# Optimization experiments

Measured on AMD Instinct MI355X. Metric: run time of the kernel, lower is better.

## Reference

```python
import jax, jax.numpy as jnp
import numpy as np

B, N, D, H = 2, 2048, 1024, 16
DK = D // H


def setup_inputs() -> dict:
    key = jax.random.key(0)
    ks = jax.random.split(key, 8)
    s = 1.0 / np.sqrt(D)  # keep projection outputs O(1)
    return {
        "x": jax.random.normal(ks[0], (B, N, D), jnp.float32),
        "alpha": jax.random.uniform(ks[1], (B, N), jnp.float32, -1.0, 1.0),
        "bias": jax.random.normal(ks[2], (B, N, N), jnp.float32) * 0.1,
        "Wq": jax.random.normal(ks[3], (D, D), jnp.float32) * s,
        "bq": jnp.zeros((D,), jnp.float32),
        "Wk": jax.random.normal(ks[4], (D, D), jnp.float32) * s,
        "bk": jnp.zeros((D,), jnp.float32),
        "Wv": jax.random.normal(ks[5], (D, D), jnp.float32) * s,
        "bv": jnp.zeros((D,), jnp.float32),
        "Wo": jax.random.normal(ks[6], (D, D), jnp.float32) * s,
        "bo": jnp.zeros((D,), jnp.float32),
    }


def reference(x, alpha, bias, Wq, bq, Wk, bk, Wv, bv, Wo, bo):
    b, n, d = x.shape
    # projections -> (B, H, N, DK)
    def split_heads(t):
        return t.reshape(b, n, H, DK).transpose(0, 2, 1, 3)

    q = split_heads(x @ Wq + bq)
    k = split_heads(x @ Wk + bk)
    v = split_heads(x @ Wv + bv)

    # salience rescale of keys/values: (B,1,N,1)
    scale = 1.0 + alpha[:, None, :, None]
    k = k * scale
    v = v * scale

    logits = jnp.einsum("bhnd,bhmd->bhnm", q, k) / np.float32(np.sqrt(DK))
    logits = logits + bias[:, None, :, :]  # broadcast over heads
    attn = jax.nn.softmax(logits, axis=-1)

    y = jnp.einsum("bhnm,bhmd->bhnd", attn, v)
    y = y.transpose(0, 2, 1, 3).reshape(b, n, d)
    return y @ Wo + bo
```

## Files before the change

### kernel.cpp

```cpp
#include <hip/hip_runtime.h>

typedef __attribute__((ext_vector_type(8))) short bf16x8;
typedef __attribute__((ext_vector_type(4))) float f32x4;

#define LOG2E 1.4426950408889634f

static __device__ __forceinline__ unsigned short f2bf(float f) {
    unsigned int u = __builtin_bit_cast(unsigned int, f);
    u += 0x7fffu + ((u >> 16) & 1u);
    return (unsigned short)(u >> 16);
}
static __device__ __forceinline__ void gload_lds16(const void* g, void* l) {
    __builtin_amdgcn_global_load_lds(
        (const __attribute__((address_space(1))) void*)g,
        (__attribute__((address_space(3))) void*)l, 16, 0, 0);
}

__launch_bounds__(256)
__global__ void prep(const float* __restrict__ x,
                     unsigned short* __restrict__ xb,
                     const float* __restrict__ W0, const float* __restrict__ W1,
                     const float* __restrict__ W2, const float* __restrict__ W3,
                     unsigned short* __restrict__ T0, unsigned short* __restrict__ T1,
                     unsigned short* __restrict__ T2, unsigned short* __restrict__ T3,
                     const float* __restrict__ bias,
                     unsigned short* __restrict__ biasP) {
    __shared__ __align__(16) float smem[8704];
    int id = blockIdx.x, tid = threadIdx.x;

    if (id < 2048) {
        int i = id * 256 + tid;
        const float4* s4 = (const float4*)x;
        float4 a = s4[2 * i], b = s4[2 * i + 1];
        uint4 u;
        u.x = (unsigned)f2bf(a.x) | ((unsigned)f2bf(a.y) << 16);
        u.y = (unsigned)f2bf(a.z) | ((unsigned)f2bf(a.w) << 16);
        u.z = (unsigned)f2bf(b.x) | ((unsigned)f2bf(b.y) << 16);
        u.w = (unsigned)f2bf(b.z) | ((unsigned)f2bf(b.w) << 16);
        *(uint4*)(xb + 8 * (size_t)i) = u;
        return;
    }
    if (id < 6144) {
        int j = id - 2048, which = j >> 10, r = j & 1023;
        const float* W = (which == 0) ? W0 : (which == 1) ? W1
                         : (which == 2) ? W2 : W3;
        unsigned short* Wt = (which == 0) ? T0 : (which == 1) ? T1
                             : (which == 2) ? T2 : T3;
        int tx = tid & 31, ty = tid >> 5;
        int x0 = (r & 31) * 32, y0 = (r >> 5) * 32;
        float* t = smem;
        for (int i = 0; i < 4; i++)
            t[(ty + 8 * i) * 33 + tx] =
                W[(size_t)(y0 + ty + 8 * i) * 1024 + x0 + tx];
        __syncthreads();
        for (int i = 0; i < 4; i++)
            Wt[(size_t)(x0 + ty + 8 * i) * 1024 + y0 + tx] =
                f2bf(t[tx * 33 + ty + 8 * i]);
        return;
    }
    {
        int j = id - 6144;
        int mt = j & 31, qt = (j >> 5) & 15, b = j >> 9;
        const float* s = bias + (size_t)b * 2048 * 2048;
        float* Ls = smem;
        for (int p = 0; p < 8; p++) {
            int row = p * 16 + (tid >> 4), f4 = tid & 15;
            float4 v = *(const float4*)
                &s[(size_t)(qt * 128 + row) * 2048 + mt * 64 + f4 * 4];
            *(float4*)&Ls[row * 68 + f4 * 4] = v;
        }
        __syncthreads();
        int w = tid >> 6, lane = tid & 63, quad = lane >> 4, l16 = lane & 15;
        unsigned short* d = biasP + (((size_t)(b * 16 + qt) * 32 + mt) * 8192);
        for (int e = 0; e < 2; e++) {
            unsigned short vals[16];
            for (int c = 0; c < 4; c++)
                for (int rr = 0; rr < 4; rr++)
                    vals[c * 4 + rr] =
                        f2bf(Ls[(e * 64 + w * 16 + quad * 4 + rr) * 68 +
                                c * 16 + l16] * LOG2E);
            unsigned short* o = d + ((size_t)((e * 4 + w) * 64 + lane)) * 16;
            *(bf16x8*)&o[0] = *(bf16x8*)&vals[0];
            *(bf16x8*)&o[8] = *(bf16x8*)&vals[8];
        }
    }
}

__launch_bounds__(256)
__global__ void gemm_qkv(const unsigned short* __restrict__ A,
                         const unsigned short* __restrict__ WqT,
                         const unsigned short* __restrict__ WkT,
                         const unsigned short* __restrict__ WvT,
                         const float* __restrict__ bq,
                         const float* __restrict__ bk,
                         const float* __restrict__ bv,
                         const float* __restrict__ alpha,
                         unsigned short* __restrict__ Qb,
                         unsigned short* __restrict__ Kb,
                         unsigned short* __restrict__ Vtb) {
    int which = blockIdx.y >> 3;
    const unsigned short* Bt = (which == 0) ? WqT : (which == 1) ? WkT : WvT;
    const float* bias = (which == 0) ? bq : (which == 1) ? bk : bv;

    __shared__ __align__(16) unsigned short As[128][64];
    __shared__ __align__(16) unsigned short Bs[128][64];
    int tid = threadIdx.x;
    int wave = tid >> 6, lane = tid & 63, quad = lane >> 4, l16 = lane & 15;
    int wm = wave & 1, wn = wave >> 1;
    int lrow = lane >> 3, lblk = lane & 7;
    int swz = ((lblk ^ lrow) * 8);
    int m0 = blockIdx.x * 128, n0 = (blockIdx.y & 7) * 128;
    f32x4 acc[4][4] = {};

    for (int kt = 0; kt < 16; kt++) {
        int k0 = kt * 64;
        for (int i = 0; i < 4; i++) {
            int rbase = i * 32 + wave * 8;
            gload_lds16(&A[(size_t)(m0 + rbase + lrow) * 1024 + k0 + swz],
                        &As[rbase][0]);
            gload_lds16(&Bt[(size_t)(n0 + rbase + lrow) * 1024 + k0 + swz],
                        &Bs[rbase][0]);
        }
        __syncthreads();
        for (int ks = 0; ks < 2; ks++) {
            int pblk = ((ks * 4 + quad) ^ (l16 & 7)) * 8;
            bf16x8 af[4], bf_[4];
            for (int i = 0; i < 4; i++)
                af[i] = *(const bf16x8*)&As[64 * wm + 16 * i + l16][pblk];
            for (int j = 0; j < 4; j++)
                bf_[j] = *(const bf16x8*)&Bs[64 * wn + 16 * j + l16][pblk];
            if (which == 2) {
                for (int i = 0; i < 4; i++)
                    for (int j = 0; j < 4; j++)
                        acc[i][j] = __builtin_amdgcn_mfma_f32_16x16x32_bf16(
                            af[i], bf_[j], acc[i][j], 0, 0, 0);
            } else {
                for (int i = 0; i < 4; i++)
                    for (int j = 0; j < 4; j++)
                        acc[i][j] = __builtin_amdgcn_mfma_f32_16x16x32_bf16(
                            bf_[j], af[i], acc[i][j], 0, 0, 0);
            }
        }
        __syncthreads();
    }

    if (which == 2) {
        for (int i = 0; i < 4; i++)
            for (int j = 0; j < 4; j++) {
                int colb = n0 + 64 * wn + 16 * j + l16;
                int h = colb >> 6, dk = colb & 63;
                int row0 = m0 + 64 * wm + 16 * i + quad * 4;
                int bb = row0 >> 11, nn0 = row0 & 2047;
                unsigned short v4[4];
                for (int r = 0; r < 4; r++) {
                    float v = acc[i][j][r] + bias[colb];
                    v4[r] = f2bf(v * (1.0f + alpha[bb * 2048 + nn0 + r]));
                }
                uint2 u;
                u.x = (unsigned)v4[0] | ((unsigned)v4[1] << 16);
                u.y = (unsigned)v4[2] | ((unsigned)v4[3] << 16);
                *(uint2*)&Vtb[((size_t)(bb * 16 + h) * 64 + dk) * 2048 + nn0] = u;
            }
    } else {
        unsigned short* outb = (which == 0) ? Qb : Kb;
        for (int i = 0; i < 4; i++)
            for (int j = 0; j < 4; j++) {
                int row = m0 + 64 * wm + 16 * i + l16;
                int bb = row >> 11, nn = row & 2047;
                int colb0 = n0 + 64 * wn + 16 * j + quad * 4;
                int h = colb0 >> 6, dk0 = colb0 & 63;
                float4 b4 = *(const float4*)&bias[colb0];
                float s = (which == 0) ? (0.125f * LOG2E)
                                       : (1.0f + alpha[bb * 2048 + nn]);
                unsigned short v4[4];
                v4[0] = f2bf((acc[i][j][0] + b4.x) * s);
                v4[1] = f2bf((acc[i][j][1] + b4.y) * s);
                v4[2] = f2bf((acc[i][j][2] + b4.z) * s);
                v4[3] = f2bf((acc[i][j][3] + b4.w) * s);
                uint2 u;
                u.x = (unsigned)v4[0] | ((unsigned)v4[1] << 16);
                u.y = (unsigned)v4[2] | ((unsigned)v4[3] << 16);
                *(uint2*)&outb[((size_t)(bb * 16 + h) * 2048 + nn) * 64 + dk0] = u;
            }
    }
}

__launch_bounds__(256)
__global__ void gemm_out(const unsigned short* __restrict__ A,
                         const unsigned short* __restrict__ Bt,
                         const float* __restrict__ bias,
                         float* __restrict__ outf) {
    __shared__ __align__(16) unsigned short As[128][64];
    __shared__ __align__(16) unsigned short Bs[128][64];
    int tid = threadIdx.x;
    int wave = tid >> 6, lane = tid & 63, quad = lane >> 4, l16 = lane & 15;
    int wm = wave & 1, wn = wave >> 1;
    int lrow = lane >> 3, lblk = lane & 7;
    int swz = ((lblk ^ lrow) * 8);
    int m0 = blockIdx.x * 128, n0 = blockIdx.y * 128;
    f32x4 acc[4][4] = {};

    for (int kt = 0; kt < 16; kt++) {
        int k0 = kt * 64;
        for (int i = 0; i < 4; i++) {
            int rbase = i * 32 + wave * 8;
            gload_lds16(&A[(size_t)(m0 + rbase + lrow) * 1024 + k0 + swz],
                        &As[rbase][0]);
            gload_lds16(&Bt[(size_t)(n0 + rbase + lrow) * 1024 + k0 + swz],
                        &Bs[rbase][0]);
        }
        __syncthreads();
        for (int ks = 0; ks < 2; ks++) {
            int pblk = ((ks * 4 + quad) ^ (l16 & 7)) * 8;
            bf16x8 af[4], bf_[4];
            for (int i = 0; i < 4; i++)
                af[i] = *(const bf16x8*)&As[64 * wm + 16 * i + l16][pblk];
            for (int j = 0; j < 4; j++)
                bf_[j] = *(const bf16x8*)&Bs[64 * wn + 16 * j + l16][pblk];
            for (int i = 0; i < 4; i++)
                for (int j = 0; j < 4; j++)
                    acc[i][j] = __builtin_amdgcn_mfma_f32_16x16x32_bf16(
                        bf_[j], af[i], acc[i][j], 0, 0, 0);
        }
        __syncthreads();
    }

    for (int i = 0; i < 4; i++)
        for (int j = 0; j < 4; j++) {
            int row = m0 + 64 * wm + 16 * i + l16;
            int colb0 = n0 + 64 * wn + 16 * j + quad * 4;
            float4 b4 = *(const float4*)&bias[colb0];
            float4 o;
            o.x = acc[i][j][0] + b4.x;
            o.y = acc[i][j][1] + b4.y;
            o.z = acc[i][j][2] + b4.z;
            o.w = acc[i][j][3] + b4.w;
            *(float4*)&outf[(size_t)row * 1024 + colb0] = o;
        }
}

__launch_bounds__(256, 4)
__global__ void attn_kernel(const unsigned short* __restrict__ Q,
                            const unsigned short* __restrict__ K,
                            const unsigned short* __restrict__ Vt,
                            const unsigned short* __restrict__ biasP,
                            unsigned short* __restrict__ Y,
                            float* __restrict__ Opart,
                            float* __restrict__ Lpart, int split) {
    __shared__ __align__(16) unsigned short Ks[64][64];
    __shared__ __align__(16) unsigned short Vs[64][64];
    __shared__ __align__(16) unsigned short Ps[4][32][72];
    int tid = threadIdx.x;
    int wave = tid >> 6, lane = tid & 63, quad = lane >> 4, l16 = lane & 15;
    int qt = blockIdx.x, h = blockIdx.y;
    int b, mt0, mtN;
    if (split) { b = blockIdx.z >> 1; int half = blockIdx.z & 1;
                 mt0 = half * 16; mtN = mt0 + 16; }
    else       { b = blockIdx.z; mt0 = 0; mtN = 32; }
    int q0 = qt * 128;
    size_t headoff = (size_t)(b * 16 + h) * 2048 * 64;
    const unsigned short* Kp = K + headoff;
    const unsigned short* Vp = Vt + headoff;
    int lrow = lane >> 3, lblk = lane & 7;
    int swz = (lblk ^ lrow) * 8;

    bf16x8 aq[2][2];
    for (int e = 0; e < 2; e++) {
        const unsigned short* qp =
            Q + headoff + (size_t)(q0 + e * 64 + wave * 16 + l16) * 64;
        aq[e][0] = *(const bf16x8*)&qp[quad * 8];
        aq[e][1] = *(const bf16x8*)&qp[32 + quad * 8];
    }
    bf16x8 ones;
    for (int j = 0; j < 8; j++) ones[j] = (short)0x3F80;

    f32x4 oacc[2][4] = {};
    f32x4 lacc[2] = {};
    const unsigned short* bP = biasP + (size_t)(b * 16 + qt) * 32 * 8192;

    for (int mt = mt0; mt < mtN; mt++) {
        int m0 = mt * 64;
        for (int i = 0; i < 2; i++) {
            int rbase = wave * 16 + i * 8;
            gload_lds16(&Kp[(size_t)(m0 + rbase + lrow) * 64 + swz], &Ks[rbase][0]);
            gload_lds16(&Vp[(size_t)(rbase + lrow) * 2048 + m0 + swz], &Vs[rbase][0]);
        }
        const unsigned short* bt = bP + (size_t)mt * 8192;
        bf16x8 bz[2][2];
        for (int e = 0; e < 2; e++) {
            const unsigned short* p = bt + (size_t)((e * 4 + wave) * 64 + lane) * 16;
            bz[e][0] = *(const bf16x8*)&p[0];
            bz[e][1] = *(const bf16x8*)&p[8];
        }
        __syncthreads();

        f32x4 sc[2][4];
        for (int e = 0; e < 2; e++)
            for (int c = 0; c < 4; c++) {
                uint2 w = ((const uint2*)&bz[e][c >> 1])[c & 1];
                f32x4 s;
                s[0] = __builtin_bit_cast(float, w.x << 16);
                s[1] = __builtin_bit_cast(float, w.x & 0xffff0000u);
                s[2] = __builtin_bit_cast(float, w.y << 16);
                s[3] = __builtin_bit_cast(float, w.y & 0xffff0000u);
                sc[e][c] = s;
            }
        __builtin_amdgcn_s_setprio(1);
        for (int c = 0; c < 4; c++) {
            for (int ks = 0; ks < 2; ks++) {
                bf16x8 kf = *(const bf16x8*)&Ks[c * 16 + l16]
                                               [((ks * 4 + quad) ^ (l16 & 7)) * 8];
                sc[0][c] = __builtin_amdgcn_mfma_f32_16x16x32_bf16(aq[0][ks], kf, sc[0][c], 0, 0, 0);
                sc[1][c] = __builtin_amdgcn_mfma_f32_16x16x32_bf16(aq[1][ks], kf, sc[1][c], 0, 0, 0);
            }
        }
        __builtin_amdgcn_s_setprio(0);

        for (int e = 0; e < 2; e++)
            for (int c = 0; c < 4; c++) {
                int colw = (((c * 2 + (l16 >> 3)) + quad) & 7) * 8 + (l16 & 7);
                for (int r = 0; r < 4; r++) {
                    float p = exp2f(sc[e][c][r]);
                    unsigned int u = __builtin_bit_cast(unsigned int, p);
                    Ps[wave][e * 16 + quad * 4 + r][colw] = (unsigned short)(u >> 16);
                }
            }

        __builtin_amdgcn_s_setprio(1);
        for (int ks = 0; ks < 2; ks++) {
            int blkr = (ks * 4 + quad + (l16 >> 2)) & 7;
            bf16x8 pf0 = *(const bf16x8*)&Ps[wave][l16][blkr * 8];
            bf16x8 pf1 = *(const bf16x8*)&Ps[wave][16 + l16][blkr * 8];
            lacc[0] = __builtin_amdgcn_mfma_f32_16x16x32_bf16(pf0, ones, lacc[0], 0, 0, 0);
            lacc[1] = __builtin_amdgcn_mfma_f32_16x16x32_bf16(pf1, ones, lacc[1], 0, 0, 0);
            for (int cv = 0; cv < 4; cv++) {
                bf16x8 vf = *(const bf16x8*)&Vs[cv * 16 + l16]
                                               [((ks * 4 + quad) ^ (l16 & 7)) * 8];
                oacc[0][cv] = __builtin_amdgcn_mfma_f32_16x16x32_bf16(pf0, vf, oacc[0][cv], 0, 0, 0);
                oacc[1][cv] = __builtin_amdgcn_mfma_f32_16x16x32_bf16(pf1, vf, oacc[1][cv], 0, 0, 0);
            }
        }
        __builtin_amdgcn_s_setprio(0);
        __syncthreads();
    }

    if (split) {
        size_t p = ((size_t)((b * 16 + h) * 16 + qt)) * 2 + (blockIdx.z & 1);
        float* Op = Opart + p * 8192;
        for (int e = 0; e < 2; e++)
            for (int cv = 0; cv < 4; cv++)
                for (int r = 0; r < 4; r++)
                    Op[(e * 64 + wave * 16 + quad * 4 + r) * 64 + cv * 16 + l16] =
                        oacc[e][cv][r];
        if (l16 == 0)
            for (int e = 0; e < 2; e++)
                for (int r = 0; r < 4; r++)
                    Lpart[p * 128 + e * 64 + wave * 16 + quad * 4 + r] = lacc[e][r];
    } else {
        for (int e = 0; e < 2; e++) {
            float invl[4];
            for (int r = 0; r < 4; r++) invl[r] = 1.0f / lacc[e][r];
            for (int cv = 0; cv < 4; cv++)
                for (int r = 0; r < 4; r++) {
                    int qrow = q0 + e * 64 + 16 * wave + quad * 4 + r;
                    int d = h * 64 + cv * 16 + l16;
                    Y[((size_t)b * 2048 + qrow) * 1024 + d] =
                        f2bf(oacc[e][cv][r] * invl[r]);
                }
        }
    }
}

__global__ void attn_combine(const float* __restrict__ Opart,
                             const float* __restrict__ Lpart,
                             unsigned short* __restrict__ Y) {
    int blk = blockIdx.x;
    int qt = blk & 15, h = (blk >> 4) & 15, b = blk >> 8;
    const float* O0 = Opart + (size_t)blk * 2 * 8192;
    const float* O1 = O0 + 8192;
    const float* L0 = Lpart + (size_t)blk * 2 * 128;
    const float* L1 = L0 + 128;
    int t = threadIdx.x;
    for (int i = 0; i < 8; i++) {
        int idx4 = i * 256 + t;
        int q = idx4 >> 4;
        int dk = (idx4 & 15) * 4;
        float4 a = *(const float4*)&O0[idx4 * 4];
        float4 c = *(const float4*)&O1[idx4 * 4];
        float inv = 1.0f / (L0[q] + L1[q]);
        uint2 u;
        u.x = (unsigned)f2bf((a.x + c.x) * inv) |
              ((unsigned)f2bf((a.y + c.y) * inv) << 16);
        u.y = (unsigned)f2bf((a.z + c.z) * inv) |
              ((unsigned)f2bf((a.w + c.w) * inv) << 16);
        int qrow = qt * 128 + q;
        *(uint2*)&Y[((size_t)b * 2048 + qrow) * 1024 + h * 64 + dk] = u;
    }
}

extern "C" void kernel_launch(void* const* d_in, const int* in_sizes, int n_in,
                              void* d_out, int out_size, void* d_ws, size_t ws_size,
                              hipStream_t stream) {
    const float* x     = (const float*)d_in[0];
    const float* alpha = (const float*)d_in[1];
    const float* bias  = (const float*)d_in[2];
    const float* Wq    = (const float*)d_in[3];
    const float* bq    = (const float*)d_in[4];
    const float* Wk    = (const float*)d_in[5];
    const float* bk    = (const float*)d_in[6];
    const float* Wv    = (const float*)d_in[7];
    const float* bv    = (const float*)d_in[8];
    const float* Wo    = (const float*)d_in[9];
    const float* bo    = (const float*)d_in[10];
    float* out = (float*)d_out;

    char* ws = (char*)d_ws;
    const size_t MB = 1048576;
    unsigned short* xb    = (unsigned short*)(ws);
    unsigned short* wqt   = (unsigned short*)(ws + 8 * MB);
    unsigned short* wkt   = (unsigned short*)(ws + 10 * MB);
    unsigned short* wvt   = (unsigned short*)(ws + 12 * MB);
    unsigned short* wot   = (unsigned short*)(ws + 14 * MB);
    unsigned short* Qb    = (unsigned short*)(ws + 16 * MB);
    unsigned short* Kb    = (unsigned short*)(ws + 24 * MB);
    unsigned short* Vtb   = (unsigned short*)(ws + 32 * MB);
    unsigned short* biasP = (unsigned short*)(ws + 40 * MB);
    float*          Opart = (float*)(ws + 56 * MB);
    float*          Lpart = (float*)(ws + 88 * MB);
    unsigned short* Yb    = xb;
    int split = (ws_size >= 90 * MB) ? 1 : 0;

    prep<<<7168, 256, 0, stream>>>(x, xb, Wq, Wk, Wv, Wo,
                                   wqt, wkt, wvt, wot, bias, biasP);

    gemm_qkv<<<dim3(32, 24), 256, 0, stream>>>(
        xb, wqt, wkt, wvt, bq, bk, bv, alpha, Qb, Kb, Vtb);

    if (split) {
        attn_kernel<<<dim3(16, 16, 4), 256, 0, stream>>>(
            Qb, Kb, Vtb, biasP, Yb, Opart, Lpart, 1);
        attn_combine<<<512, 256, 0, stream>>>(Opart, Lpart, Yb);
    } else {
        attn_kernel<<<dim3(16, 16, 2), 256, 0, stream>>>(
            Qb, Kb, Vtb, biasP, Yb, Opart, Lpart, 0);
    }

    gemm_out<<<dim3(32, 8), 256, 0, stream>>>(Yb, wot, bo, out);
}
```

Baseline: 244.0 us.

## Move bias repacking into QKV GEMM launch and halve output GEMM tile width

The bias-to-bf16 MFMA-layout repacking moves out of the prep kernel into extra blocks of the QKV GEMM grid. Those blocks convert to bf16 before staging in LDS, so they use less shared memory, and the prep kernel's large shared buffer shrinks to a 32x33 tile. The output GEMM tile drops from 128x128 to 128x64, which doubles its grid to 512 blocks so the CUs are better filled. The costs are a shared-memory footprint in gemm_qkv sized for the GEMM tiles and less reuse of A per block in the output GEMM.

```diff
diff --git a/kernel.cpp b/kernel.cpp
--- a/kernel.cpp
+++ b/kernel.cpp
@@ -22,10 +22,7 @@
                      const float* __restrict__ W0, const float* __restrict__ W1,
                      const float* __restrict__ W2, const float* __restrict__ W3,
                      unsigned short* __restrict__ T0, unsigned short* __restrict__ T1,
-                     unsigned short* __restrict__ T2, unsigned short* __restrict__ T3,
-                     const float* __restrict__ bias,
-                     unsigned short* __restrict__ biasP) {
-    __shared__ __align__(16) float smem[8704];
+                     unsigned short* __restrict__ T2, unsigned short* __restrict__ T3) {
     int id = blockIdx.x, tid = threadIdx.x;
 
     if (id < 2048) {
@@ -40,7 +37,8 @@
         *(uint4*)(xb + 8 * (size_t)i) = u;
         return;
     }
-    if (id < 6144) {
+    {
+        __shared__ float t[32][33];
         int j = id - 2048, which = j >> 10, r = j & 1023;
         const float* W = (which == 0) ? W0 : (which == 1) ? W1
                          : (which == 2) ? W2 : W3;
@@ -48,41 +46,12 @@
                              : (which == 2) ? T2 : T3;
         int tx = tid & 31, ty = tid >> 5;
         int x0 = (r & 31) * 32, y0 = (r >> 5) * 32;
-        float* t = smem;
         for (int i = 0; i < 4; i++)
-            t[(ty + 8 * i) * 33 + tx] =
-                W[(size_t)(y0 + ty + 8 * i) * 1024 + x0 + tx];
+            t[ty + 8 * i][tx] = W[(size_t)(y0 + ty + 8 * i) * 1024 + x0 + tx];
         __syncthreads();
         for (int i = 0; i < 4; i++)
             Wt[(size_t)(x0 + ty + 8 * i) * 1024 + y0 + tx] =
-                f2bf(t[tx * 33 + ty + 8 * i]);
-        return;
-    }
-    {
-        int j = id - 6144;
-        int mt = j & 31, qt = (j >> 5) & 15, b = j >> 9;
-        const float* s = bias + (size_t)b * 2048 * 2048;
-        float* Ls = smem;
-        for (int p = 0; p < 8; p++) {
-            int row = p * 16 + (tid >> 4), f4 = tid & 15;
-            float4 v = *(const float4*)
-                &s[(size_t)(qt * 128 + row) * 2048 + mt * 64 + f4 * 4];
-            *(float4*)&Ls[row * 68 + f4 * 4] = v;
-        }
-        __syncthreads();
-        int w = tid >> 6, lane = tid & 63, quad = lane >> 4, l16 = lane & 15;
-        unsigned short* d = biasP + (((size_t)(b * 16 + qt) * 32 + mt) * 8192);
-        for (int e = 0; e < 2; e++) {
-            unsigned short vals[16];
-            for (int c = 0; c < 4; c++)
-                for (int rr = 0; rr < 4; rr++)
-                    vals[c * 4 + rr] =
-                        f2bf(Ls[(e * 64 + w * 16 + quad * 4 + rr) * 68 +
-                                c * 16 + l16] * LOG2E);
-            unsigned short* o = d + ((size_t)((e * 4 + w) * 64 + lane)) * 16;
-            *(bf16x8*)&o[0] = *(bf16x8*)&vals[0];
-            *(bf16x8*)&o[8] = *(bf16x8*)&vals[8];
-        }
+                f2bf(t[tx][ty + 8 * i]);
     }
 }
 
@@ -95,16 +64,49 @@
                          const float* __restrict__ bk,
                          const float* __restrict__ bv,
                          const float* __restrict__ alpha,
+                         const float* __restrict__ bias2d,
+                         unsigned short* __restrict__ biasP,
                          unsigned short* __restrict__ Qb,
                          unsigned short* __restrict__ Kb,
                          unsigned short* __restrict__ Vtb) {
+    __shared__ __align__(16) unsigned short sh[16384];
+    int tid = threadIdx.x;
+
+    if (blockIdx.y >= 24) {
+        int id = blockIdx.x + 32 * (blockIdx.y - 24);
+        int mt = id & 31, qt = (id >> 5) & 15, b = id >> 9;
+        const float* s = bias2d + (size_t)b * 2048 * 2048;
+        for (int p = 0; p < 8; p++) {
+            int row = p * 16 + (tid >> 4), f4 = tid & 15;
+            float4 v = *(const float4*)
+                &s[(size_t)(qt * 128 + row) * 2048 + mt * 64 + f4 * 4];
+            uint2 u;
+            u.x = (unsigned)f2bf(v.x * LOG2E) | ((unsigned)f2bf(v.y * LOG2E) << 16);
+            u.y = (unsigned)f2bf(v.z * LOG2E) | ((unsigned)f2bf(v.w * LOG2E) << 16);
+            *(uint2*)&sh[row * 68 + f4 * 4] = u;
+        }
+        __syncthreads();
+        int w = tid >> 6, lane = tid & 63, quad = lane >> 4, l16 = lane & 15;
+        unsigned short* d = biasP + (((size_t)(b * 16 + qt) * 32 + mt) * 8192);
+        for (int e = 0; e < 2; e++) {
+            unsigned short vals[16];
+            for (int c = 0; c < 4; c++)
+                for (int rr = 0; rr < 4; rr++)
+                    vals[c * 4 + rr] =
+                        sh[(e * 64 + w * 16 + quad * 4 + rr) * 68 + c * 16 + l16];
+            unsigned short* o = d + ((size_t)((e * 4 + w) * 64 + lane)) * 16;
+            *(bf16x8*)&o[0] = *(bf16x8*)&vals[0];
+            *(bf16x8*)&o[8] = *(bf16x8*)&vals[8];
+        }
+        return;
+    }
+
+    unsigned short (*As)[64] = (unsigned short(*)[64])sh;
+    unsigned short (*Bs)[64] = (unsigned short(*)[64])(sh + 8192);
     int which = blockIdx.y >> 3;
     const unsigned short* Bt = (which == 0) ? WqT : (which == 1) ? WkT : WvT;
     const float* bias = (which == 0) ? bq : (which == 1) ? bk : bv;
 
-    __shared__ __align__(16) unsigned short As[128][64];
-    __shared__ __align__(16) unsigned short Bs[128][64];
-    int tid = threadIdx.x;
     int wave = tid >> 6, lane = tid & 63, quad = lane >> 4, l16 = lane & 15;
     int wm = wave & 1, wn = wave >> 1;
     int lrow = lane >> 3, lblk = lane & 7;
@@ -191,14 +193,14 @@
                          const float* __restrict__ bias,
                          float* __restrict__ outf) {
     __shared__ __align__(16) unsigned short As[128][64];
-    __shared__ __align__(16) unsigned short Bs[128][64];
+    __shared__ __align__(16) unsigned short Bs[64][64];
     int tid = threadIdx.x;
     int wave = tid >> 6, lane = tid & 63, quad = lane >> 4, l16 = lane & 15;
     int wm = wave & 1, wn = wave >> 1;
     int lrow = lane >> 3, lblk = lane & 7;
     int swz = ((lblk ^ lrow) * 8);
-    int m0 = blockIdx.x * 128, n0 = blockIdx.y * 128;
-    f32x4 acc[4][4] = {};
+    int m0 = blockIdx.x * 128, n0 = blockIdx.y * 64;
+    f32x4 acc[4][2] = {};
 
     for (int kt = 0; kt < 16; kt++) {
         int k0 = kt * 64;
@@ -206,19 +208,22 @@
             int rbase = i * 32 + wave * 8;
             gload_lds16(&A[(size_t)(m0 + rbase + lrow) * 1024 + k0 + swz],
                         &As[rbase][0]);
+        }
+        for (int i = 0; i < 2; i++) {
+            int rbase = i * 32 + wave * 8;
             gload_lds16(&Bt[(size_t)(n0 + rbase + lrow) * 1024 + k0 + swz],
                         &Bs[rbase][0]);
         }
         __syncthreads();
         for (int ks = 0; ks < 2; ks++) {
             int pblk = ((ks * 4 + quad) ^ (l16 & 7)) * 8;
-            bf16x8 af[4], bf_[4];
+            bf16x8 af[4], bf_[2];
             for (int i = 0; i < 4; i++)
                 af[i] = *(const bf16x8*)&As[64 * wm + 16 * i + l16][pblk];
-            for (int j = 0; j < 4; j++)
-                bf_[j] = *(const bf16x8*)&Bs[64 * wn + 16 * j + l16][pblk];
+            for (int j = 0; j < 2; j++)
+                bf_[j] = *(const bf16x8*)&Bs[32 * wn + 16 * j + l16][pblk];
             for (int i = 0; i < 4; i++)
-                for (int j = 0; j < 4; j++)
+                for (int j = 0; j < 2; j++)
                     acc[i][j] = __builtin_amdgcn_mfma_f32_16x16x32_bf16(
                         bf_[j], af[i], acc[i][j], 0, 0, 0);
         }
@@ -226,9 +231,9 @@
     }
 
     for (int i = 0; i < 4; i++)
-        for (int j = 0; j < 4; j++) {
+        for (int j = 0; j < 2; j++) {
             int row = m0 + 64 * wm + 16 * i + l16;
-            int colb0 = n0 + 64 * wn + 16 * j + quad * 4;
+            int colb0 = n0 + 32 * wn + 16 * j + quad * 4;
             float4 b4 = *(const float4*)&bias[colb0];
             float4 o;
             o.x = acc[i][j][0] + b4.x;
@@ -430,11 +435,10 @@
     unsigned short* Yb    = xb;
     int split = (ws_size >= 90 * MB) ? 1 : 0;
 
-    prep<<<7168, 256, 0, stream>>>(x, xb, Wq, Wk, Wv, Wo,
-                                   wqt, wkt, wvt, wot, bias, biasP);
-
-    gemm_qkv<<<dim3(32, 24), 256, 0, stream>>>(
-        xb, wqt, wkt, wvt, bq, bk, bv, alpha, Qb, Kb, Vtb);
+    prep<<<6144, 256, 0, stream>>>(x, xb, Wq, Wk, Wv, Wo, wqt, wkt, wvt, wot);
+
+    gemm_qkv<<<dim3(32, 56), 256, 0, stream>>>(
+        xb, wqt, wkt, wvt, bq, bk, bv, alpha, bias, biasP, Qb, Kb, Vtb);
 
     if (split) {
         attn_kernel<<<dim3(16, 16, 4), 256, 0, stream>>>(
@@ -445,5 +449,5 @@
             Qb, Kb, Vtb, biasP, Yb, Opart, Lpart, 0);
     }
 
-    gemm_out<<<dim3(32, 8), 256, 0, stream>>>(Yb, wot, bo, out);
-}
+    gemm_out<<<dim3(32, 16), 256, 0, stream>>>(Yb, wot, bo, out);
+}
```

Result: faster. 235.7 us (-3.4%).
